# Performance work log

Measured on AMD Instinct MI355X. Metric: run time of the kernel, lower is better.

## Reference

```python
import jax, jax.numpy as jnp
import numpy as np

NUM_VAR = 20000   # variables
D = 8             # domain size per variable
NUM_VAL = NUM_VAR * D
NUM_CST = 20000   # constraints
DEG = 8           # values per constraint
NUM_E = NUM_CST * DEG
H = 128           # hidden_dim
STEPS = 4


def setup_inputs() -> dict:
    key = jax.random.key(0)
    ks = jax.random.split(key, 16)
    s = 0.1 / np.sqrt(H)
    w = lambda k, shape: jax.random.normal(k, shape, jnp.float32) * s
    inp = dict(
        h_val_init=jax.random.normal(ks[0], (1, H), jnp.float32),
        W1=w(ks[1], (H + 1, H)), b1=jnp.zeros((H,), jnp.float32),
        W2=w(ks[2], (H, H)),
        Wx=w(ks[3], (H, H)), bx=jnp.zeros((H,), jnp.float32),
        Wc=w(ks[4], (2 * H, H)), bc=jnp.zeros((H,), jnp.float32),
        Wv=w(ks[5], (2 * H, H)), bv=jnp.zeros((H,), jnp.float32),
        Wi=w(ks[6], (H, 3 * H)), Wh=w(ks[7], (H, 3 * H)),
        bi=jnp.zeros((3 * H,), jnp.float32), bh=jnp.zeros((3 * H,), jnp.float32),
        Wp1=w(ks[8], (H, H)), bp1=jnp.zeros((H,), jnp.float32),
        Wp2=w(ks[9], (H, 1)),
    )
    u = jax.random.uniform(ks[10], (STEPS + 1, NUM_VAL), jnp.float32, 1e-6, 1.0 - 1e-6)
    inp['gumbel'] = -jnp.log(-jnp.log(u))  # Gumbel(0,1) noise: one draw per sampling event
    inp['val_idx'] = jax.random.randint(ks[11], (NUM_E,), 0, NUM_VAL, jnp.int32)
    inp['cst_idx'] = jnp.repeat(jnp.arange(NUM_CST, dtype=jnp.int32), DEG)
    inp['steps'] = STEPS
    return inp


def _gru(x, h, Wi, Wh, bi, bh):
    gi = x @ Wi + bi
    gh = h @ Wh + bh
    ir, iz, inn = jnp.split(gi, 3, axis=1)
    hr, hz, hn = jnp.split(gh, 3, axis=1)
    r = jax.nn.sigmoid(ir + hr)
    z = jax.nn.sigmoid(iz + hz)
    n = jnp.tanh(inn + r * hn)
    return (1.0 - z) * n + z * h


def reference(h_val_init, W1, b1, W2, Wx, bx, Wc, bc, Wv, bv, Wi, Wh, bi, bh,
              Wp1, bp1, Wp2, gumbel, val_idx, cst_idx, steps):
    def sample(logits, g):
        lg = logits.reshape(NUM_VAR, D)
        logp = jax.nn.log_softmax(lg, axis=1)
        choice = jnp.argmax(lg + g.reshape(NUM_VAR, D), axis=1)  # Gumbel-max categorical sample
        assign = jax.nn.one_hot(choice, D, dtype=jnp.float32).reshape(NUM_VAL)
        lp = jnp.sum(jnp.take_along_axis(logp, choice[:, None], axis=1))
        return assign, lp

    def num_unsat(assign):
        # constraint satisfied if any incident value is currently assigned
        sat = jax.ops.segment_max(assign[val_idx], cst_idx, num_segments=NUM_CST)
        return jnp.float32(NUM_CST) - jnp.sum(sat)

    # init_assignment: uniform logits -> pure Gumbel argmax
    assign0, _ = sample(jnp.zeros((NUM_VAL,), jnp.float32), gumbel[0])
    best0 = num_unsat(assign0)
    h0 = jnp.tile(h_val_init, (NUM_VAL, 1))

    def step(carry, g):
        h_val, assign, best = carry
        # val2cst: gather value states + assignment bit, edge MLP, scatter to constraints
        a_e = assign[val_idx][:, None]                                   # [E,1]
        m = jax.nn.relu(jnp.concatenate([h_val[val_idx], a_e], axis=1) @ W1 + b1) @ W2
        r_cst = jax.ops.segment_sum(m, cst_idx, num_segments=NUM_CST)    # [C,H]
        x_val = jax.nn.relu(h_val @ Wx + bx)                             # [V,H]
        # cst2val: gather constraint messages back, scatter to values
        y_e = jax.nn.relu(jnp.concatenate([r_cst[cst_idx], x_val[val_idx]], axis=1) @ Wc + bc)
        y_val = jax.ops.segment_sum(y_e, val_idx, num_segments=NUM_VAL)  # [V,H]
        # val2val: aggregate within each variable's domain
        y_r = y_val.reshape(NUM_VAR, D, H)
        agg = jnp.broadcast_to(y_r.mean(axis=1, keepdims=True), y_r.shape)
        z = jax.nn.relu(jnp.concatenate([y_r, agg], axis=2).reshape(NUM_VAL, 2 * H) @ Wv + bv)
        h_val = _gru(z, h_val, Wi, Wh, bi, bh)
        logits = (jax.nn.relu(h_val @ Wp1 + bp1) @ Wp2)[:, 0]            # policy -> [V]
        assign, lp = sample(logits, g)
        nu = num_unsat(assign)
        best = jnp.minimum(best, nu)
        return (h_val, assign, best), (lp, nu)

    (h_val, assign, best), (log_probs, unsat_per_step) = jax.lax.scan(
        step, (h0, assign0, best0), gumbel[1:])
    return log_probs, unsat_per_step, best
```

## Files before the change

kernel.cpp:

```cpp
#include <hip/hip_runtime.h>
#include <math.h>

#define NVAR  20000
#define NVAL  160000
#define NCST  20000
#define NEDGE 160000
#define HD    128
#define NT16  10000

typedef __attribute__((ext_vector_type(8))) short  short8;
typedef __attribute__((ext_vector_type(4))) float  f32x4;
typedef __attribute__((ext_vector_type(4))) float  floatx4;

static __device__ __forceinline__ float sigf(float x) {
    return __fdividef(1.0f, 1.0f + __expf(-x));
}
static __device__ __forceinline__ float tanhf_(float x) {
    return 1.0f - __fdividef(2.0f, 1.0f + __expf(2.0f * x));
}

static __device__ __forceinline__ short bf16c(float f) {
    unsigned u = __float_as_uint(f);
    u += 0x7fffu + ((u >> 16) & 1u);
    return (short)(u >> 16);
}
static __device__ __forceinline__ float bf2f(unsigned short b) {
    return __uint_as_float(((unsigned)b) << 16);
}
static __device__ __forceinline__ short8 pack8(floatx4 a, floatx4 b) {
    short8 r;
    r[0] = bf16c(a[0]); r[1] = bf16c(a[1]); r[2] = bf16c(a[2]); r[3] = bf16c(a[3]);
    r[4] = bf16c(b[0]); r[5] = bf16c(b[1]); r[6] = bf16c(b[2]); r[7] = bf16c(b[3]);
    return r;
}

struct WD  { const float* W; short* WT; int K; int N; int total; };
struct WDs { WD d[7]; };

__global__ __launch_bounds__(256) void k_wconv7(WDs ds) {
    WD d = ds.d[blockIdx.y];
    int i = blockIdx.x * 256 + threadIdx.x;
    if (i >= d.total) return;
    int n = i / d.K, k = i - n * d.K;
    d.WT[i] = bf16c(d.W[(size_t)k * d.N + n]);
}

__global__ __launch_bounds__(256) void k_w2c(const float* __restrict__ W2,
                                             const float* __restrict__ Wc,
                                             short* __restrict__ W2cT) {
    int i = blockIdx.x * 256 + threadIdx.x;
    int n = i >> 7, k = i & 127;
    float s = 0.f;
    for (int m = 0; m < 128; ++m) s += W2[k * 128 + m] * Wc[m * 128 + n];
    W2cT[n * 128 + k] = bf16c(s);
}

__global__ __launch_bounds__(256) void k_hist(const int* __restrict__ val_idx,
                                              int* __restrict__ deg) {
    int e = blockIdx.x * 256 + threadIdx.x;
    if (e < NEDGE) atomicAdd(&deg[val_idx[e]], 1);
}
__global__ __launch_bounds__(256) void k_scan1(const int* __restrict__ deg,
                                               int* __restrict__ bsum) {
    __shared__ int s[256];
    int i = blockIdx.x * 256 + threadIdx.x;
    s[threadIdx.x] = deg[i];
    __syncthreads();
    for (int o = 128; o > 0; o >>= 1) {
        if (threadIdx.x < o) s[threadIdx.x] += s[threadIdx.x + o];
        __syncthreads();
    }
    if (threadIdx.x == 0) bsum[blockIdx.x] = s[0];
}
__global__ void k_scan2(const int* __restrict__ bsum, int* __restrict__ boff, int nb) {
    if (threadIdx.x == 0 && blockIdx.x == 0) {
        int acc = 0;
        for (int b = 0; b < nb; ++b) { boff[b] = acc; acc += bsum[b]; }
        boff[nb] = acc;
    }
}
__global__ __launch_bounds__(256) void k_scan3(const int* __restrict__ deg,
                                               const int* __restrict__ boff,
                                               int* __restrict__ off,
                                               int* __restrict__ cursor) {
    __shared__ int s[256];
    int i = blockIdx.x * 256 + threadIdx.x;
    int d = deg[i];
    s[threadIdx.x] = d;
    __syncthreads();
    for (int o = 1; o < 256; o <<= 1) {
        int v = s[threadIdx.x];
        if (threadIdx.x >= o) v += s[threadIdx.x - o];
        __syncthreads();
        s[threadIdx.x] = v;
        __syncthreads();
    }
    int excl = s[threadIdx.x] - d + boff[blockIdx.x];
    off[i] = excl;
    cursor[i] = excl;
    if (i == NVAL - 1) off[NVAL] = NEDGE;
}
__global__ __launch_bounds__(256) void k_place(const int* __restrict__ val_idx,
                                               int* __restrict__ cursor,
                                               int* __restrict__ inv) {
    int e = blockIdx.x * 256 + threadIdx.x;
    if (e < NEDGE) {
        int p = atomicAdd(&cursor[val_idx[e]], 1);
        inv[p] = e >> 3;
    }
}

__global__ __launch_bounds__(256) void k_init_hb(short* __restrict__ h,
                                                 const float* __restrict__ hinit) {
    size_t i = (size_t)blockIdx.x * 256 + threadIdx.x;
    h[i] = bf16c(hinit[i & (HD - 1)]);
}

__global__ __launch_bounds__(256) void k_sample0(const float* __restrict__ g,
                                                 float* __restrict__ assign,
                                                 float* __restrict__ lp_accum) {
    int v = blockIdx.x * 256 + threadIdx.x;
    float lp = 0.f;
    if (v < NVAR) {
        int choice = 0;
        float bestv = -1e30f;
#pragma unroll
        for (int d = 0; d < 8; ++d) {
            float t = g[v * 8 + d];
            if (t > bestv) { bestv = t; choice = d; }
        }
        lp = -__logf(8.0f);
#pragma unroll
        for (int d = 0; d < 8; ++d) assign[v * 8 + d] = (d == choice) ? 1.f : 0.f;
    }
    __shared__ float sred[256];
    sred[threadIdx.x] = lp;
    __syncthreads();
    for (int o = 128; o > 0; o >>= 1) {
        if (threadIdx.x < o) sred[threadIdx.x] += sred[threadIdx.x + o];
        __syncthreads();
    }
    if (threadIdx.x == 0) atomicAdd(lp_accum, sred[0]);
}

__global__ __launch_bounds__(256) void k_unsat(const float* __restrict__ assign,
                                               const int* __restrict__ val_idx,
                                               int* __restrict__ sat_accum) {
    int c = blockIdx.x * 256 + threadIdx.x;
    int sat = 0;
    if (c < NCST) {
#pragma unroll
        for (int j = 0; j < 8; ++j)
            if (assign[val_idx[c * 8 + j]] > 0.5f) sat = 1;
    }
    __shared__ int sred[256];
    sred[threadIdx.x] = sat;
    __syncthreads();
    for (int o = 128; o > 0; o >>= 1) {
        if (threadIdx.x < o) sred[threadIdx.x] += sred[threadIdx.x + o];
        __syncthreads();
    }
    if (threadIdx.x == 0) atomicAdd(sat_accum, sred[0]);
}

__global__ void k_finalize(const float* __restrict__ lp, const int* __restrict__ sat,
                           float* __restrict__ best, float* __restrict__ out,
                           int s, int S, int mode) {
    float nu = (float)NCST - (float)(*sat);
    if (mode == 0) {
        *best = nu;
    } else {
        out[s] = *lp;
        out[S + s] = nu;
        float b = *best;
        if (nu < b) b = nu;
        *best = b;
        if (s == S - 1) out[2 * S] = b;
    }
}

__global__ void k_report(float* out, float v) {
    for (int i = 0; i < 9; ++i) out[i] = v;
}

static constexpr int AM_DIRECT = 1, AM_GATHER = 2;
static constexpr int EPI_STORE = 0, EPI_RCST = 1;

template <int A0M, bool BIT, bool RELU, int EPI>
__global__ __launch_bounds__(256)
void k_gemmA(const short* __restrict__ A, const int* __restrict__ aidx,
             const float* __restrict__ abit, const float* __restrict__ w1r128,
             const short* __restrict__ WT, const float* __restrict__ bias0,
             short* __restrict__ outBF, short* __restrict__ rcstOut,
             int nrows) {
    const int tid  = threadIdx.x;
    const int w    = tid >> 6;
    const int lane = tid & 63;
    const int li   = lane & 15;
    const int hi   = lane >> 4;

    __shared__ short blds[128 * 136];
    for (int c2 = tid; c2 < 2048; c2 += 256) {
        int r = c2 >> 4, off = c2 & 15;
        *(short8*)(blds + r * 136 + off * 8) = *(const short8*)(WT + (size_t)r * 128 + off * 8);
    }
    __syncthreads();

    float bv[8];
#pragma unroll
    for (int t = 0; t < 8; ++t) bv[t] = bias0 ? bias0[t * 16 + li] : 0.f;
    float wv[8];
    if constexpr (BIT) {
#pragma unroll
        for (int t = 0; t < 8; ++t) wv[t] = w1r128[t * 16 + li];
    }

    const int nt = nrows >> 4;
    const int stride = gridDim.x * 4;
    for (int rt = blockIdx.x * 4 + w; rt < nt; rt += stride) {
        const int ar = rt * 16 + li;
        int ia = ar;
        if constexpr (A0M == AM_GATHER) ia = aidx[ar];
        const short8* arow = (const short8*)(A + (size_t)ia * HD);

        short8 af[4];
#pragma unroll
        for (int kc = 0; kc < 4; ++kc) af[kc] = arow[kc * 4 + hi];

        f32x4 acc[8];
#pragma unroll
        for (int t = 0; t < 8; ++t) acc[t] = (f32x4){0.f, 0.f, 0.f, 0.f};
#pragma unroll
        for (int kc = 0; kc < 4; ++kc)
#pragma unroll
            for (int t = 0; t < 8; ++t) {
                short8 bf = *(const short8*)(blds + (t * 16 + li) * 136 + kc * 32 + hi * 8);
                acc[t] = __builtin_amdgcn_mfma_f32_16x16x32_bf16(af[kc], bf, acc[t], 0, 0, 0);
            }

        if constexpr (BIT) {
#pragma unroll
            for (int r = 0; r < 4; ++r) {
                int gr = rt * 16 + hi * 4 + r;
                float bitv = abit[aidx[gr]];
#pragma unroll
                for (int t = 0; t < 8; ++t) acc[t][r] += bitv * wv[t];
            }
        }
#pragma unroll
        for (int t = 0; t < 8; ++t)
#pragma unroll
            for (int r = 0; r < 4; ++r) {
                acc[t][r] += bv[t];
                if constexpr (RELU) acc[t][r] = fmaxf(acc[t][r], 0.f);
            }

        if constexpr (EPI == EPI_STORE) {
#pragma unroll
            for (int r = 0; r < 4; ++r) {
                int gr = rt * 16 + hi * 4 + r;
                short* o = outBF + (size_t)gr * HD + li;
#pragma unroll
                for (int t = 0; t < 8; ++t) o[t * 16] = bf16c(acc[t][r]);
            }
        } else {
#pragma unroll
            for (int t = 0; t < 8; ++t) {
                float s = acc[t][0] + acc[t][1] + acc[t][2] + acc[t][3];
                s += __shfl_xor(s, 16);
                if (hi == 0)      rcstOut[(size_t)(rt * 2) * HD + t * 16 + li]     = bf16c(s);
                else if (hi == 2) rcstOut[(size_t)(rt * 2 + 1) * HD + t * 16 + li] = bf16c(s);
            }
        }
    }
}

__global__ __launch_bounds__(256)
void k_gather(const short* __restrict__ r2c, const short* __restrict__ uV,
              const int* __restrict__ off, const int* __restrict__ inv,
              const float* __restrict__ bcv, short* __restrict__ yV) {
    const int w    = threadIdx.x >> 6;
    const int lane = threadIdx.x & 63;
    const int c0   = lane * 2;

    const float b0 = bcv[c0], b1 = bcv[c0 + 1];

    for (int v = blockIdx.x * 4 + w; v < NVAL; v += gridDim.x * 4) {
        const int e0 = off[v], e1 = off[v + 1];
        unsigned uu = *(const unsigned*)(uV + (size_t)v * HD + c0);
        const float u0 = bf2f((unsigned short)(uu & 0xffffu)) + b0;
        const float u1 = bf2f((unsigned short)(uu >> 16)) + b1;
        float a0 = 0.f, a1 = 0.f;
        for (int e = e0; e < e1; ++e) {
            const int cst = inv[e];
            unsigned rv = *(const unsigned*)(r2c + (size_t)cst * HD + c0);
            a0 += fmaxf(bf2f((unsigned short)(rv & 0xffffu)) + u0, 0.f);
            a1 += fmaxf(bf2f((unsigned short)(rv >> 16)) + u1, 0.f);
        }
        unsigned o = (unsigned)(unsigned short)bf16c(a0) |
                     ((unsigned)(unsigned short)bf16c(a1) << 16);
        *(unsigned*)(yV + (size_t)v * HD + c0) = o;
    }
}

__global__ __launch_bounds__(256)
void k_gemmZ8(const short* __restrict__ yV, const short* __restrict__ WvT,
              const float* __restrict__ bvv, short* __restrict__ outT) {
    const int tid  = threadIdx.x;
    const int w    = tid >> 6;
    const int lane = tid & 63;
    const int li   = lane & 15;
    const int hi   = lane >> 4;
    const int ch   = blockIdx.x >> 10;
    const int rba  = blockIdx.x & 1023;

    __shared__ short blds[64 * 264];
    for (int c2 = tid; c2 < 2048; c2 += 256) {
        int r = c2 >> 5, off = c2 & 31;
        *(short8*)(blds + r * 264 + off * 8) =
            *(const short8*)(WvT + (size_t)(ch * 64 + r) * 256 + off * 8);
    }
    __syncthreads();

    float bv[4];
#pragma unroll
    for (int t = 0; t < 4; ++t) bv[t] = bvv[ch * 64 + t * 16 + li];

    for (int rt = rba * 4 + w; rt < NT16; rt += 4096) {
        const int v = rt * 16 + li;
        const short8* yr = (const short8*)(yV + (size_t)v * HD);

        short8 af[8];
        floatx4 m[8];
#pragma unroll
        for (int kc = 0; kc < 4; ++kc) {
            short8 yv = yr[kc * 4 + hi];
            af[kc] = yv;
#pragma unroll
            for (int j = 0; j < 4; ++j) {
                m[2 * kc][j]     = bf2f((unsigned short)yv[j]);
                m[2 * kc + 1][j] = bf2f((unsigned short)yv[4 + j]);
            }
        }
#pragma unroll
        for (int q = 0; q < 8; ++q)
#pragma unroll
            for (int e2 = 0; e2 < 4; ++e2) {
                m[q][e2] += __shfl_xor(m[q][e2], 1);
                m[q][e2] += __shfl_xor(m[q][e2], 2);
                m[q][e2] += __shfl_xor(m[q][e2], 4);
                m[q][e2] *= 0.125f;
            }
#pragma unroll
        for (int kc = 0; kc < 4; ++kc) af[4 + kc] = pack8(m[2 * kc], m[2 * kc + 1]);

        f32x4 acc[4];
#pragma unroll
        for (int t = 0; t < 4; ++t) acc[t] = (f32x4){0.f, 0.f, 0.f, 0.f};
#pragma unroll
        for (int kc = 0; kc < 8; ++kc)
#pragma unroll
            for (int t = 0; t < 4; ++t) {
                short8 bf = *(const short8*)(blds + (t * 16 + li) * 264 + kc * 32 + hi * 8);
                acc[t] = __builtin_amdgcn_mfma_f32_16x16x32_bf16(af[kc], bf, acc[t], 0, 0, 0);
            }

#pragma unroll
        for (int r = 0; r < 4; ++r) {
            int gr = rt * 16 + hi * 4 + r;
            short* o = outT + (size_t)gr * HD + ch * 64 + li;
#pragma unroll
            for (int t = 0; t < 4; ++t)
                o[t * 16] = bf16c(fmaxf(acc[t][r] + bv[t], 0.f));
        }
    }
}

__global__ __launch_bounds__(256)
void k_gruL(const short* __restrict__ Z, const short* __restrict__ Hold,
            short* __restrict__ Hnew,
            const short* __restrict__ WiT, const short* __restrict__ WhT,
            const float* __restrict__ bi, const float* __restrict__ bh) {
    const int tid  = threadIdx.x;
    const int w    = tid >> 6;
    const int lane = tid & 63;
    const int li   = lane & 15;
    const int hi   = lane >> 4;
    const int g    = blockIdx.x >> 8;
    const int rba  = blockIdx.x & 255;

    __shared__ short blds[96 * 136];
    for (int c2 = tid; c2 < 1536; c2 += 256) {
        int r = c2 >> 4, off = c2 & 15;
        int r2 = (r < 48) ? r : r - 48;
        int sl = r2 >> 4, l = r2 & 15;
        const short* src = ((r < 48) ? WiT : WhT) + (size_t)(sl * 128 + g * 16 + l) * 128 + off * 8;
        *(short8*)(blds + r * 136 + off * 8) = *(const short8*)src;
    }
    __syncthreads();

    const int c = g * 16 + li;
    const float bR  = bi[c] + bh[c];
    const float bZg = bi[128 + c] + bh[128 + c];
    const float bIN = bi[256 + c];
    const float bHN = bh[256 + c];

    const int stride = 1024;
    int rt = rba * 4 + w;
    short8 zf[4], hf[4];
    if (rt < NT16) {
        const short8* zr = (const short8*)(Z    + (size_t)(rt * 16 + li) * HD);
        const short8* hr = (const short8*)(Hold + (size_t)(rt * 16 + li) * HD);
#pragma unroll
        for (int kc = 0; kc < 4; ++kc) { zf[kc] = zr[kc * 4 + hi]; hf[kc] = hr[kc * 4 + hi]; }
    }
    while (rt < NT16) {
        const int rtn = rt + stride;

        f32x4 aR = {0.f,0.f,0.f,0.f}, aZ = {0.f,0.f,0.f,0.f};
        f32x4 aN = {0.f,0.f,0.f,0.f}, aH = {0.f,0.f,0.f,0.f};
#pragma unroll
        for (int kc = 0; kc < 4; ++kc) {
            const int ko = kc * 32 + hi * 8;
            short8 b0 = *(const short8*)(blds + (     li) * 136 + ko);
            short8 b1 = *(const short8*)(blds + (16 + li) * 136 + ko);
            short8 b2 = *(const short8*)(blds + (32 + li) * 136 + ko);
            aR = __builtin_amdgcn_mfma_f32_16x16x32_bf16(zf[kc], b0, aR, 0, 0, 0);
            aZ = __builtin_amdgcn_mfma_f32_16x16x32_bf16(zf[kc], b1, aZ, 0, 0, 0);
            aN = __builtin_amdgcn_mfma_f32_16x16x32_bf16(zf[kc], b2, aN, 0, 0, 0);
        }
#pragma unroll
        for (int kc = 0; kc < 4; ++kc) {
            const int ko = kc * 32 + hi * 8;
            short8 b0 = *(const short8*)(blds + (48 +      li) * 136 + ko);
            short8 b1 = *(const short8*)(blds + (48 + 16 + li) * 136 + ko);
            short8 b2 = *(const short8*)(blds + (48 + 32 + li) * 136 + ko);
            aR = __builtin_amdgcn_mfma_f32_16x16x32_bf16(hf[kc], b0, aR, 0, 0, 0);
            aZ = __builtin_amdgcn_mfma_f32_16x16x32_bf16(hf[kc], b1, aZ, 0, 0, 0);
            aH = __builtin_amdgcn_mfma_f32_16x16x32_bf16(hf[kc], b2, aH, 0, 0, 0);
        }

        short8 zfn[4], hfn[4];
        const bool vn = rtn < NT16;
        if (vn) {
            const short8* zr = (const short8*)(Z    + (size_t)(rtn * 16 + li) * HD);
            const short8* hr = (const short8*)(Hold + (size_t)(rtn * 16 + li) * HD);
#pragma unroll
            for (int kc = 0; kc < 4; ++kc) { zfn[kc] = zr[kc * 4 + hi]; hfn[kc] = hr[kc * 4 + hi]; }
        }

#pragma unroll
        for (int r = 0; r < 4; ++r) {
            int gr = rt * 16 + hi * 4 + r;
            float hv = bf2f(((const unsigned short*)Hold)[(size_t)gr * HD + c]);
            float rr = sigf(aR[r] + bR);
            float zz = sigf(aZ[r] + bZg);
            float nn = tanhf_(aN[r] + bIN + rr * (aH[r] + bHN));
            Hnew[(size_t)gr * HD + c] = bf16c((1.f - zz) * nn + zz * hv);
        }

        if (vn) {
#pragma unroll
            for (int kc = 0; kc < 4; ++kc) { zf[kc] = zfn[kc]; hf[kc] = hfn[kc]; }
        }
        rt = rtn;
    }
}

__global__ __launch_bounds__(256)
void k_polS(const short* __restrict__ H, const short* __restrict__ Wp1T,
            const float* __restrict__ bp1, const float* __restrict__ Wp2,
            const float* __restrict__ gum_t, float* __restrict__ assign,
            float* __restrict__ lp_acc) {
    const int tid  = threadIdx.x;
    const int w    = tid >> 6;
    const int lane = tid & 63;
    const int li   = lane & 15;
    const int hi   = lane >> 4;

    __shared__ short blds[128 * 136];
    for (int c2 = tid; c2 < 2048; c2 += 256) {
        int r = c2 >> 4, off = c2 & 15;
        *(short8*)(blds + r * 136 + off * 8) = *(const short8*)(Wp1T + (size_t)r * 128 + off * 8);
    }
    __syncthreads();

    float bv[8], wpv[8];
#pragma unroll
    for (int t = 0; t < 8; ++t) { bv[t] = bp1[t * 16 + li]; wpv[t] = Wp2[t * 16 + li]; }

    float lpSum = 0.f;
    const int stride = gridDim.x * 4;
    for (int rt = blockIdx.x * 4 + w; rt < NT16; rt += stride) {
        const short8* arow = (const short8*)(H + (size_t)(rt * 16 + li) * HD);
        short8 af[4];
#pragma unroll
        for (int kc = 0; kc < 4; ++kc) af[kc] = arow[kc * 4 + hi];

        f32x4 acc[8];
#pragma unroll
        for (int t = 0; t < 8; ++t) acc[t] = (f32x4){0.f, 0.f, 0.f, 0.f};
#pragma unroll
        for (int kc = 0; kc < 4; ++kc)
#pragma unroll
            for (int t = 0; t < 8; ++t) {
                short8 bf = *(const short8*)(blds + (t * 16 + li) * 136 + kc * 32 + hi * 8);
                acc[t] = __builtin_amdgcn_mfma_f32_16x16x32_bf16(af[kc], bf, acc[t], 0, 0, 0);
            }

        float lg[4];
#pragma unroll
        for (int r = 0; r < 4; ++r) {
            float p = 0.f;
#pragma unroll
            for (int t = 0; t < 8; ++t) p = fmaf(fmaxf(acc[t][r] + bv[t], 0.f), wpv[t], p);
            p += __shfl_xor(p, 1);
            p += __shfl_xor(p, 2);
            p += __shfl_xor(p, 4);
            p += __shfl_xor(p, 8);
            lg[r] = p;
        }

        float bt = -1e30f, bl = 0.f; int bd = 0;
#pragma unroll
        for (int r = 0; r < 4; ++r) {
            float tv = lg[r] + gum_t[rt * 16 + hi * 4 + r];
            int d = (hi & 1) * 4 + r;
            if (tv > bt) { bt = tv; bl = lg[r]; bd = d; }
        }
        float ot = __shfl_xor(bt, 16);
        float ol = __shfl_xor(bl, 16);
        int   od = __shfl_xor(bd, 16);
        if (ot > bt || (ot == bt && od < bd)) { bt = ot; bl = ol; bd = od; }

        float mx = fmaxf(fmaxf(lg[0], lg[1]), fmaxf(lg[2], lg[3]));
        mx = fmaxf(mx, __shfl_xor(mx, 16));
        float se = __expf(lg[0] - mx) + __expf(lg[1] - mx) +
                   __expf(lg[2] - mx) + __expf(lg[3] - mx);
        se += __shfl_xor(se, 16);

        if (li == 0) {
#pragma unroll
            for (int r = 0; r < 4; ++r)
                assign[rt * 16 + hi * 4 + r] = ((hi & 1) * 4 + r == bd) ? 1.f : 0.f;
            if ((hi & 1) == 0) lpSum += bl - mx - __logf(se);
        }
    }

    __shared__ float sred[256];
    sred[tid] = lpSum;
    __syncthreads();
    for (int o = 128; o > 0; o >>= 1) {
        if (tid < o) sred[tid] += sred[tid + o];
        __syncthreads();
    }
    if (tid == 0) atomicAdd(lp_acc, sred[0]);
}

extern "C" void kernel_launch(void* const* d_in, const int* in_sizes, int n_in,
                              void* d_out, int out_size, void* d_ws, size_t ws_size,
                              hipStream_t stream) {
    const float* h_init = (const float*)d_in[0];
    const float* W1  = (const float*)d_in[1];
    const float* b1  = (const float*)d_in[2];
    const float* W2  = (const float*)d_in[3];
    const float* Wx  = (const float*)d_in[4];
    const float* bx  = (const float*)d_in[5];
    const float* Wc  = (const float*)d_in[6];
    const float* bc  = (const float*)d_in[7];
    const float* Wv  = (const float*)d_in[8];
    const float* bv  = (const float*)d_in[9];
    const float* Wi  = (const float*)d_in[10];
    const float* Wh  = (const float*)d_in[11];
    const float* bi  = (const float*)d_in[12];
    const float* bh  = (const float*)d_in[13];
    const float* Wp1 = (const float*)d_in[14];
    const float* bp1 = (const float*)d_in[15];
    const float* Wp2 = (const float*)d_in[16];
    const float* gum = (const float*)d_in[17];
    const int* val_idx = (const int*)d_in[18];
    float* out = (float*)d_out;

    const int S = (out_size - 1) / 2;

    const size_t VH = (size_t)NVAL * HD;
    short* hbA   = (short*)d_ws;
    short* hbB   = hbA + VH;
    short* tA    = hbB + VH;
    short* uV    = tA + VH;
    short* yV    = uV + VH;
    short* s_cst = yV + VH;
    short* r2c   = s_cst + (size_t)NCST * HD;
    short* W1T  = r2c + (size_t)NCST * HD;
    short* W2cT = W1T  + 16384;
    short* WxT  = W2cT + 16384;
    short* Wp1T = WxT  + 16384;
    short* WcBT = Wp1T + 16384;
    short* WvT  = WcBT + 16384;
    short* WiT  = WvT  + 32768;
    short* WhT  = WiT  + 49152;
    float* assign = (float*)(WhT + 49152);
    float* lp_acc = assign + NVAL;
    int*   sat    = (int*)(lp_acc + 8);
    float* best   = (float*)(sat + 8);
    int*   deg    = (int*)(best + 8);
    int*   off    = deg + NVAL;
    int*   cursor = off + NVAL + 1;
    int*   inv    = cursor + NVAL;
    int*   bsum   = inv + NEDGE;
    int*   boff   = bsum + 625;

    const size_t needed = (size_t)((char*)(boff + 626) - (char*)d_ws);
    if (ws_size < needed) {
        k_report<<<1, 1, 0, stream>>>(out, (float)ws_size);
        return;
    }

    WDs ds;
    ds.d[0] = { W1,            W1T,  128, 128, 16384 };
    ds.d[1] = { Wx,            WxT,  128, 128, 16384 };
    ds.d[2] = { Wp1,           Wp1T, 128, 128, 16384 };
    ds.d[3] = { Wc + 128*128,  WcBT, 128, 128, 16384 };
    ds.d[4] = { Wv,            WvT,  256, 128, 32768 };
    ds.d[5] = { Wi,            WiT,  128, 384, 49152 };
    ds.d[6] = { Wh,            WhT,  128, 384, 49152 };
    k_wconv7<<<dim3(192, 7), dim3(256), 0, stream>>>(ds);
    k_w2c<<<dim3(64), dim3(256), 0, stream>>>(W2, Wc, W2cT);

    (void)hipMemsetAsync(lp_acc, 0, 24 * sizeof(float), stream);
    (void)hipMemsetAsync(deg, 0, (size_t)NVAL * sizeof(int), stream);
    k_hist <<<dim3(625), dim3(256), 0, stream>>>(val_idx, deg);
    k_scan1<<<dim3(625), dim3(256), 0, stream>>>(deg, bsum);
    k_scan2<<<1, 1, 0, stream>>>(bsum, boff, 625);
    k_scan3<<<dim3(625), dim3(256), 0, stream>>>(deg, boff, off, cursor);
    k_place<<<dim3(625), dim3(256), 0, stream>>>(val_idx, cursor, inv);

    const dim3 B256(256);
    const dim3 gA(1280);
    const dim3 gW(320);
    const dim3 gB(2048);
    const dim3 gG(2048);
    const dim3 gS(2048);
    const dim3 gVar((NVAR + 255) / 256);
    const float* w1r128 = W1 + (size_t)128 * HD;

    k_init_hb<<<dim3(NVAL * HD / 256), B256, 0, stream>>>(hbA, h_init);
    k_sample0<<<gVar, B256, 0, stream>>>(gum, assign, lp_acc);
    k_unsat<<<gVar, B256, 0, stream>>>(assign, val_idx, sat);
    k_finalize<<<1, 1, 0, stream>>>(lp_acc, sat, best, out, 0, S, 0);

    for (int s = 0; s < S; ++s) {
        const int t = s + 1;
        const short* hcur = (s & 1) ? hbB : hbA;
        short*       hnxt = (s & 1) ? hbA : hbB;
        k_gemmA<AM_GATHER, true, true, EPI_RCST><<<gA, B256, 0, stream>>>(
            hcur, val_idx, assign, w1r128, W1T, b1, nullptr, s_cst, NVAL);
        k_gemmA<AM_DIRECT, false, false, EPI_STORE><<<gW, B256, 0, stream>>>(
            s_cst, nullptr, nullptr, nullptr, W2cT, nullptr, r2c, nullptr, NCST);
        k_gemmA<AM_DIRECT, false, true, EPI_STORE><<<gA, B256, 0, stream>>>(
            hcur, nullptr, nullptr, nullptr, WxT, bx, tA, nullptr, NVAL);
        k_gemmA<AM_DIRECT, false, false, EPI_STORE><<<gA, B256, 0, stream>>>(
            tA, nullptr, nullptr, nullptr, WcBT, nullptr, uV, nullptr, NVAL);
        k_gather<<<gS, B256, 0, stream>>>(r2c, uV, off, inv, bc, yV);
        k_gemmZ8<<<gB, B256, 0, stream>>>(yV, WvT, bv, tA);
        k_gruL<<<gG, B256, 0, stream>>>(tA, hcur, hnxt, WiT, WhT, bi, bh);
        k_polS<<<gA, B256, 0, stream>>>(hnxt, Wp1T, bp1, Wp2,
                                        gum + (size_t)t * NVAL, assign, lp_acc + t);
        k_unsat<<<gVar, B256, 0, stream>>>(assign, val_idx, sat + t);
        k_finalize<<<1, 1, 0, stream>>>(lp_acc + t, sat + t, best, out, s, S, 1);
    }
}
```

Measured before the change: 1.275 ms.

## Fuse Wx and Wc-bottom GEMMs into one back-to-back MFMA kernel

Replaces two separate GEMM launches (h@Wx+relu into tA, then tA@WcB into uV) with a single kernel that keeps the intermediate activation in registers. The first GEMM's accumulator is repacked directly as the second GEMM's A operand, and Wc is pre-permuted on the host side of the pipeline to match that register layout. This removes a full NVAL x 128 bf16 write and read of the intermediate plus one launch per step. It also reorders block index decoding in gemmZ8 and gruL so that adjacent blocks share row tiles, which may improve L2 locality. The fused kernel uses about 68KB of LDS and many registers, which could limit occupancy.

Measured after the change: 1.210 ms. 5.1% less time.

```diff
diff --git a/kernel.cpp b/kernel.cpp
--- a/kernel.cpp
+++ b/kernel.cpp
@@ -35,9 +35,9 @@
 }
 
 struct WD  { const float* W; short* WT; int K; int N; int total; };
-struct WDs { WD d[7]; };
-
-__global__ __launch_bounds__(256) void k_wconv7(WDs ds) {
+struct WDs { WD d[6]; };
+
+__global__ __launch_bounds__(256) void k_wconv6(WDs ds) {
     WD d = ds.d[blockIdx.y];
     int i = blockIdx.x * 256 + threadIdx.x;
     if (i >= d.total) return;
@@ -53,6 +53,15 @@
     float s = 0.f;
     for (int m = 0; m < 128; ++m) s += W2[k * 128 + m] * Wc[m * 128 + n];
     W2cT[n * 128 + k] = bf16c(s);
+}
+
+__global__ __launch_bounds__(256) void k_wcbp(const float* __restrict__ Wc,
+                                              short* __restrict__ WcBP) {
+    int i = blockIdx.x * 256 + threadIdx.x;
+    int n2 = i >> 7, s = i & 127;
+    int kc = s >> 5, rem = s & 31, hi2 = rem >> 3, j = rem & 7;
+    int k = (kc * 2 + (j >> 2)) * 16 + hi2 * 4 + (j & 3);
+    WcBP[n2 * 128 + s] = bf16c(Wc[(size_t)(128 + k) * 128 + n2]);
 }
 
 __global__ __launch_bounds__(256) void k_hist(const int* __restrict__ val_idx,
@@ -276,6 +285,81 @@
 }
 
 __global__ __launch_bounds__(256)
+void k_gemmXU(const short* __restrict__ H, const short* __restrict__ WxT,
+              const short* __restrict__ WcBP, const float* __restrict__ bx,
+              short* __restrict__ uV) {
+    const int tid  = threadIdx.x;
+    const int w    = tid >> 6;
+    const int lane = tid & 63;
+    const int li   = lane & 15;
+    const int hi   = lane >> 4;
+
+    __shared__ short wx[128 * 136];
+    __shared__ short wc[128 * 136];
+    for (int c2 = tid; c2 < 2048; c2 += 256) {
+        int r = c2 >> 4, off = c2 & 15;
+        *(short8*)(wx + r * 136 + off * 8) = *(const short8*)(WxT  + (size_t)r * 128 + off * 8);
+        *(short8*)(wc + r * 136 + off * 8) = *(const short8*)(WcBP + (size_t)r * 128 + off * 8);
+    }
+    __syncthreads();
+
+    float bx32[8][4];
+#pragma unroll
+    for (int t = 0; t < 8; ++t)
+#pragma unroll
+        for (int r = 0; r < 4; ++r) bx32[t][r] = bx[t * 16 + hi * 4 + r];
+
+    const int stride = gridDim.x * 4;
+    for (int rt = blockIdx.x * 4 + w; rt < NT16; rt += stride) {
+        const short8* arow = (const short8*)(H + (size_t)(rt * 16 + li) * HD);
+        short8 af[4];
+#pragma unroll
+        for (int kc = 0; kc < 4; ++kc) af[kc] = arow[kc * 4 + hi];
+
+        f32x4 a1[8];
+#pragma unroll
+        for (int t = 0; t < 8; ++t) a1[t] = (f32x4){0.f, 0.f, 0.f, 0.f};
+#pragma unroll
+        for (int kc = 0; kc < 4; ++kc)
+#pragma unroll
+            for (int t = 0; t < 8; ++t) {
+                short8 wf = *(const short8*)(wx + (t * 16 + li) * 136 + kc * 32 + hi * 8);
+                a1[t] = __builtin_amdgcn_mfma_f32_16x16x32_bf16(wf, af[kc], a1[t], 0, 0, 0);
+            }
+
+        floatx4 xv[8];
+#pragma unroll
+        for (int t = 0; t < 8; ++t)
+#pragma unroll
+            for (int r = 0; r < 4; ++r)
+                xv[t][r] = fmaxf(a1[t][r] + bx32[t][r], 0.f);
+
+        short8 af2[4];
+#pragma unroll
+        for (int kc = 0; kc < 4; ++kc) af2[kc] = pack8(xv[2 * kc], xv[2 * kc + 1]);
+
+        f32x4 a2[8];
+#pragma unroll
+        for (int t = 0; t < 8; ++t) a2[t] = (f32x4){0.f, 0.f, 0.f, 0.f};
+#pragma unroll
+        for (int kc = 0; kc < 4; ++kc)
+#pragma unroll
+            for (int t = 0; t < 8; ++t) {
+                short8 bf = *(const short8*)(wc + (t * 16 + li) * 136 + kc * 32 + hi * 8);
+                a2[t] = __builtin_amdgcn_mfma_f32_16x16x32_bf16(af2[kc], bf, a2[t], 0, 0, 0);
+            }
+
+#pragma unroll
+        for (int r = 0; r < 4; ++r) {
+            int gr = rt * 16 + hi * 4 + r;
+            short* o = uV + (size_t)gr * HD + li;
+#pragma unroll
+            for (int t = 0; t < 8; ++t) o[t * 16] = bf16c(a2[t][r]);
+        }
+    }
+}
+
+__global__ __launch_bounds__(256)
 void k_gather(const short* __restrict__ r2c, const short* __restrict__ uV,
               const int* __restrict__ off, const int* __restrict__ inv,
               const float* __restrict__ bcv, short* __restrict__ yV) {
@@ -311,8 +395,8 @@
     const int lane = tid & 63;
     const int li   = lane & 15;
     const int hi   = lane >> 4;
-    const int ch   = blockIdx.x >> 10;
-    const int rba  = blockIdx.x & 1023;
+    const int ch   = blockIdx.x & 1;
+    const int rba  = blockIdx.x >> 1;
 
     __shared__ short blds[64 * 264];
     for (int c2 = tid; c2 < 2048; c2 += 256) {
@@ -386,8 +470,8 @@
     const int lane = tid & 63;
     const int li   = lane & 15;
     const int hi   = lane >> 4;
-    const int g    = blockIdx.x >> 8;
-    const int rba  = blockIdx.x & 255;
+    const int g    = blockIdx.x & 7;
+    const int rba  = blockIdx.x >> 3;
 
     __shared__ short blds[96 * 136];
     for (int c2 = tid; c2 < 1536; c2 += 256) {
@@ -595,8 +679,8 @@
     short* W2cT = W1T  + 16384;
     short* WxT  = W2cT + 16384;
     short* Wp1T = WxT  + 16384;
-    short* WcBT = Wp1T + 16384;
-    short* WvT  = WcBT + 16384;
+    short* WcBP = Wp1T + 16384;
+    short* WvT  = WcBP + 16384;
     short* WiT  = WvT  + 32768;
     short* WhT  = WiT  + 49152;
     float* assign = (float*)(WhT + 49152);
@@ -617,15 +701,15 @@
     }
 
     WDs ds;
-    ds.d[0] = { W1,            W1T,  128, 128, 16384 };
-    ds.d[1] = { Wx,            WxT,  128, 128, 16384 };
-    ds.d[2] = { Wp1,           Wp1T, 128, 128, 16384 };
-    ds.d[3] = { Wc + 128*128,  WcBT, 128, 128, 16384 };
-    ds.d[4] = { Wv,            WvT,  256, 128, 32768 };
-    ds.d[5] = { Wi,            WiT,  128, 384, 49152 };
-    ds.d[6] = { Wh,            WhT,  128, 384, 49152 };
-    k_wconv7<<<dim3(192, 7), dim3(256), 0, stream>>>(ds);
-    k_w2c<<<dim3(64), dim3(256), 0, stream>>>(W2, Wc, W2cT);
+    ds.d[0] = { W1,  W1T,  128, 128, 16384 };
+    ds.d[1] = { Wx,  WxT,  128, 128, 16384 };
+    ds.d[2] = { Wp1, Wp1T, 128, 128, 16384 };
+    ds.d[3] = { Wv,  WvT,  256, 128, 32768 };
+    ds.d[4] = { Wi,  WiT,  128, 384, 49152 };
+    ds.d[5] = { Wh,  WhT,  128, 384, 49152 };
+    k_wconv6<<<dim3(192, 6), dim3(256), 0, stream>>>(ds);
+    k_w2c <<<dim3(64), dim3(256), 0, stream>>>(W2, Wc, W2cT);
+    k_wcbp<<<dim3(64), dim3(256), 0, stream>>>(Wc, WcBP);
 
     (void)hipMemsetAsync(lp_acc, 0, 24 * sizeof(float), stream);
     (void)hipMemsetAsync(deg, 0, (size_t)NVAL * sizeof(int), stream);
@@ -638,6 +722,7 @@
     const dim3 B256(256);
     const dim3 gA(1280);
     const dim3 gW(320);
+    const dim3 gXU(512);
     const dim3 gB(2048);
     const dim3 gG(2048);
     const dim3 gS(2048);
@@ -657,10 +742,7 @@
             hcur, val_idx, assign, w1r128, W1T, b1, nullptr, s_cst, NVAL);
         k_gemmA<AM_DIRECT, false, false, EPI_STORE><<<gW, B256, 0, stream>>>(
             s_cst, nullptr, nullptr, nullptr, W2cT, nullptr, r2c, nullptr, NCST);
-        k_gemmA<AM_DIRECT, false, true, EPI_STORE><<<gA, B256, 0, stream>>>(
-            hcur, nullptr, nullptr, nullptr, WxT, bx, tA, nullptr, NVAL);
-        k_gemmA<AM_DIRECT, false, false, EPI_STORE><<<gA, B256, 0, stream>>>(
-            tA, nullptr, nullptr, nullptr, WcBT, nullptr, uV, nullptr, NVAL);
+        k_gemmXU<<<gXU, B256, 0, stream>>>(hcur, WxT, WcBP, bx, uV);
         k_gather<<<gS, B256, 0, stream>>>(r2c, uV, off, inv, bc, yV);
         k_gemmZ8<<<gB, B256, 0, stream>>>(yV, WvT, bv, tA);
         k_gruL<<<gG, B256, 0, stream>>>(tA, hcur, hnxt, WiT, WhT, bi, bh);
```
